# Kernel optimization log

Measured on AMD Instinct MI355X. Metric: run time of the kernel, lower is better.

The kernel has to match this reference:

```python
import jax, jax.numpy as jnp
import numpy as np

D_MODEL = 2048
NHEADS = 16
HEAD_DIM = D_MODEL // NHEADS


def setup_inputs() -> dict:
    key = jax.random.key(0)
    kx, kq, kk, kv, ko = jax.random.split(key, 5)
    B, S = 2, 2048
    scale = 1.0 / np.sqrt(D_MODEL)
    return {
        "x": jax.random.normal(kx, (B, S, D_MODEL), dtype=jnp.float32),
        "Wq": jax.random.normal(kq, (D_MODEL, D_MODEL), dtype=jnp.float32) * scale,
        "Wk": jax.random.normal(kk, (D_MODEL, D_MODEL), dtype=jnp.float32) * scale,
        "Wv": jax.random.normal(kv, (D_MODEL, D_MODEL), dtype=jnp.float32) * scale,
        "Wo": jax.random.normal(ko, (D_MODEL, D_MODEL), dtype=jnp.float32) * scale,
    }


def reference(x, Wq, Wk, Wv, Wo):
    B, S, _ = x.shape
    # nn.Linear(bias=False): y = x @ W.T
    q = (x @ Wq.T).reshape(B, S, NHEADS, HEAD_DIM)
    k = (x @ Wk.T).reshape(B, S, NHEADS, HEAD_DIM)
    v = (x @ Wv.T).reshape(B, S, NHEADS, HEAD_DIM)
    sm_scale = 1.0 / np.sqrt(HEAD_DIM)
    # scores: [B, H, S, S]
    scores = jnp.einsum("bqhd,bkhd->bhqk", q, k) * sm_scale
    causal_mask = jnp.tril(jnp.ones((S, S), dtype=bool))  # [S, S]
    scores = jnp.where(causal_mask, scores, jnp.finfo(scores.dtype).min)
    probs = jax.nn.softmax(scores, axis=-1)
    attn = jnp.einsum("bhqk,bkhd->bqhd", probs, v)  # [B, S, H, D]
    out = attn.reshape(B, S, D_MODEL) @ Wo.T
    return out
```

## Files before the change

kernel.cpp:

```cpp
#include <hip/hip_runtime.h>
#include <hip/hip_bf16.h>
#include <type_traits>

#define DEV __device__ __forceinline__

typedef __bf16 bf16x8 __attribute__((ext_vector_type(8)));
typedef float f32x4 __attribute__((ext_vector_type(4)));
typedef float f32x16 __attribute__((ext_vector_type(16)));
typedef unsigned short u16;
typedef unsigned int u32;

DEV u16 f32_to_bf16(float f) {
  union { float f; u32 u; } x; x.f = f;
  u32 r = (x.u + 0x7FFFu + ((x.u >> 16) & 1u)) >> 16;
  return (u16)r;
}

DEV u32 pack2(float a, float b) {
  union { __hip_bfloat162 h; u32 u; } c;
  c.h = __float22bfloat162_rn(float2{a, b});
  return c.u;
}

DEV void ld_lds16(const void* g, void* l) {
  __builtin_amdgcn_global_load_lds(
      (const __attribute__((address_space(1))) u32*)g,
      (__attribute__((address_space(3))) u32*)l, 16, 0, 0);
}

#define MFMA16(a, b, c) __builtin_amdgcn_mfma_f32_16x16x32_bf16(a, b, c, 0, 0, 0)
#define MFMA32(a, b, c) __builtin_amdgcn_mfma_f32_32x32x16_bf16(a, b, c, 0, 0, 0)

__global__ __launch_bounds__(256) void cast_all(
    const float* __restrict__ x,  const float* __restrict__ wq,
    const float* __restrict__ wk, const float* __restrict__ wv,
    const float* __restrict__ wo,
    u16* __restrict__ xb,  u16* __restrict__ wqb, u16* __restrict__ wkb,
    u16* __restrict__ wvb, u16* __restrict__ wob) {
  int bid = blockIdx.x;
  const float* src; u16* dst; int base;
  if (bid < 8192)       { src = x;  dst = xb;  base = bid; }
  else if (bid < 12288) { src = wq; dst = wqb; base = bid - 8192; }
  else if (bid < 16384) { src = wk; dst = wkb; base = bid - 12288; }
  else if (bid < 20480) { src = wv; dst = wvb; base = bid - 16384; }
  else                  { src = wo; dst = wob; base = bid - 20480; }
  int i = (base * 256 + threadIdx.x) * 4;
  float4 v = *reinterpret_cast<const float4*>(src + i);
  ushort4 o;
  o.x = f32_to_bf16(v.x); o.y = f32_to_bf16(v.y);
  o.z = f32_to_bf16(v.z); o.w = f32_to_bf16(v.w);
  *reinterpret_cast<ushort4*>(dst + i) = o;
}

template <typename OutT>
__global__ __launch_bounds__(512, 2) void gemm_nt256(
    const u16* __restrict__ A, const u16* __restrict__ B, OutT* __restrict__ C,
    int M, int N, int K, float oscLo, float oscHi, int nsplit, int nbx) {
  __shared__ __align__(16) u16 sA[2][256 * 64];
  __shared__ __align__(16) u16 sB[2][256 * 64];
  const int tid = threadIdx.x;
  const int lane = tid & 63, wid = tid >> 6;
  const int l31 = lane & 31, hi5 = lane >> 5;
  const int wm = wid >> 2, wn = wid & 3;
  const int cpx = gridDim.x >> 3;
  const int swz = ((int)blockIdx.x & 7) * cpx + ((int)blockIdx.x >> 3);
  const int m0 = (swz / nbx) * 256, n0 = (swz % nbx) * 256;
  const int NT = K >> 6;

  f32x16 acc[4][2] = {};

  auto stage = [&](int buf, int t) {
    const int k0 = t << 6;
#pragma unroll
    for (int i = 0; i < 4; ++i) {
      int e = i * 512 + tid;
      int r = e >> 3;
      int bc = ((e & 7) * 16) ^ ((r & 7) << 4);
      ld_lds16(A + (size_t)(m0 + r) * K + k0 + (bc >> 1), &sA[buf][e * 8]);
    }
#pragma unroll
    for (int i = 0; i < 4; ++i) {
      int e = i * 512 + tid;
      int r = e >> 3;
      int bc = ((e & 7) * 16) ^ ((r & 7) << 4);
      ld_lds16(B + (size_t)(n0 + r) * K + k0 + (bc >> 1), &sB[buf][e * 8]);
    }
  };

  stage(0, 0);
  __syncthreads();

  for (int t = 0; t < NT; ++t) {
    const u16* cA = sA[t & 1];
    const u16* cB = sB[t & 1];
    if (t + 1 < NT) stage((t + 1) & 1, t + 1);

#pragma unroll
    for (int kh = 0; kh < 2; ++kh) {
      bf16x8 afr[4][2], bfr[2][2];
#pragma unroll
      for (int mi = 0; mi < 4; ++mi)
#pragma unroll
        for (int kc = 0; kc < 2; ++kc) {
          int row = wm * 128 + mi * 32 + l31;
          int bo = (((kh * 2 + kc) * 32 + hi5 * 16)) ^ ((row & 7) << 4);
          afr[mi][kc] = *(const bf16x8*)((const char*)cA + row * 128 + bo);
        }
#pragma unroll
      for (int ni = 0; ni < 2; ++ni)
#pragma unroll
        for (int kc = 0; kc < 2; ++kc) {
          int row = wn * 64 + ni * 32 + l31;
          int bo = (((kh * 2 + kc) * 32 + hi5 * 16)) ^ ((row & 7) << 4);
          bfr[ni][kc] = *(const bf16x8*)((const char*)cB + row * 128 + bo);
        }
      asm volatile("s_waitcnt lgkmcnt(0)" ::: "memory");
      __builtin_amdgcn_sched_barrier(0);
      __builtin_amdgcn_s_setprio(1);
#pragma unroll
      for (int mi = 0; mi < 4; ++mi)
#pragma unroll
        for (int ni = 0; ni < 2; ++ni)
#pragma unroll
          for (int kc = 0; kc < 2; ++kc)
            acc[mi][ni] = MFMA32(afr[mi][kc], bfr[ni][kc], acc[mi][ni]);
      __builtin_amdgcn_s_setprio(0);
      __builtin_amdgcn_sched_barrier(0);
    }
    __syncthreads();
  }

#pragma unroll
  for (int mi = 0; mi < 4; ++mi)
#pragma unroll
    for (int ni = 0; ni < 2; ++ni) {
      int colb = n0 + wn * 64 + ni * 32;
      float osc = (colb < nsplit) ? oscLo : oscHi;
      int col = colb + l31;
#pragma unroll
      for (int j = 0; j < 16; ++j) {
        size_t row = m0 + wm * 128 + mi * 32 + (j & 3) + 8 * (j >> 2) + 4 * hi5;
        float v = acc[mi][ni][j] * osc;
        if constexpr (std::is_same<OutT, float>::value)
          C[row * N + col] = v;
        else
          C[row * N + col] = f32_to_bf16(v);
      }
    }
}

template <typename OutT>
__global__ __launch_bounds__(256) void gemm_nt(const u16* __restrict__ A,
                                               const u16* __restrict__ B,
                                               OutT* __restrict__ C,
                                               int M, int N, int K,
                                               float oscLo, float oscHi, int nsplit) {
  __shared__ __align__(16) u16 sA[128 * 64];
  __shared__ __align__(16) u16 sB[128 * 64];
  const int tid = threadIdx.x;
  const int lane = tid & 63, wid = tid >> 6;
  const int lo = lane & 15, hi = lane >> 4;
  const int wm = wid >> 1, wn = wid & 1;
  const int m0 = blockIdx.y * 128, n0 = blockIdx.x * 128;
  const float osc = (n0 < nsplit) ? oscLo : oscHi;

  f32x4 acc[4][4] = {};

  for (int k0 = 0; k0 < K; k0 += 64) {
    __syncthreads();
#pragma unroll
    for (int i = 0; i < 4; ++i) {
      int e16 = i * 256 + tid;
      int r = e16 >> 3;
      int bcol = ((e16 & 7) * 16) ^ ((r & 7) << 4);
      int col = bcol >> 1;
      ld_lds16(A + (size_t)(m0 + r) * K + k0 + col, sA + e16 * 8);
      ld_lds16(B + (size_t)(n0 + r) * K + k0 + col, sB + e16 * 8);
    }
    __syncthreads();
#pragma unroll
    for (int kc = 0; kc < 2; ++kc) {
      bf16x8 a[4], b[4];
#pragma unroll
      for (int i = 0; i < 4; ++i) {
        int row = wm * 64 + i * 16 + lo;
        int boff = ((kc * 32 + hi * 8) * 2) ^ ((row & 7) << 4);
        a[i] = *(const bf16x8*)((const char*)sA + row * 128 + boff);
      }
#pragma unroll
      for (int i = 0; i < 4; ++i) {
        int row = wn * 64 + i * 16 + lo;
        int boff = ((kc * 32 + hi * 8) * 2) ^ ((row & 7) << 4);
        b[i] = *(const bf16x8*)((const char*)sB + row * 128 + boff);
      }
#pragma unroll
      for (int mi = 0; mi < 4; ++mi)
#pragma unroll
        for (int ni = 0; ni < 4; ++ni)
          acc[mi][ni] = MFMA16(a[mi], b[ni], acc[mi][ni]);
    }
  }
#pragma unroll
  for (int mi = 0; mi < 4; ++mi)
#pragma unroll
    for (int r = 0; r < 4; ++r) {
      size_t row = m0 + wm * 64 + mi * 16 + hi * 4 + r;
#pragma unroll
      for (int ni = 0; ni < 4; ++ni) {
        int col = n0 + wn * 64 + ni * 16 + lo;
        float v = acc[mi][ni][r] * osc;
        if constexpr (std::is_same<OutT, float>::value)
          C[row * N + col] = v;
        else
          C[row * N + col] = f32_to_bf16(v);
      }
    }
}

constexpr float RTHR2 = 11.5416f;

__global__ __launch_bounds__(256, 2) void attn_fwd(const u16* __restrict__ QK,
                                                   const u16* __restrict__ VT,
                                                   u16* __restrict__ O) {
  __shared__ __align__(16) u16 sK[2][64 * 128];
  __shared__ __align__(16) u16 sV[2][128 * 64];

  const int x = blockIdx.x, h = blockIdx.y, b = blockIdx.z;
  const int qt = b ? x : (15 - x);
  const int tid = threadIdx.x;
  const int lane = tid & 63, wid = tid >> 6;
  const int l31 = lane & 31, hi5 = lane >> 5;

  const size_t baseQ = ((size_t)b * 2048) * 4096 + (size_t)h * 128;
  const size_t baseK = baseQ + 2048;
  const size_t baseV = ((size_t)h * 128) * 4096 + (size_t)b * 2048;
  const int q0 = qt * 128;
  const int qw = q0 + wid * 32;
  const int qg = qw + l31;
  const int nt = 2 * qt + 2;

  bf16x8 qf[8];
#pragma unroll
  for (int kc = 0; kc < 8; ++kc)
    qf[kc] = *(const bf16x8*)(QK + baseQ + (size_t)qg * 4096 + kc * 16 + hi5 * 8);

  f32x16 o[4] = {};
  float m = -INFINITY, ls = 0.f;

  auto stage = [&](int buf, int t) {
    const int kv = t * 64;
#pragma unroll
    for (int i = 0; i < 4; ++i) {
      int e = i * 256 + tid;
      int r = e >> 4;
      int bc = ((e & 15) * 16) ^ ((r & 7) << 4);
      ld_lds16(QK + baseK + (size_t)(kv + r) * 4096 + (bc >> 1), &sK[buf][e * 8]);
    }
#pragma unroll
    for (int i = 0; i < 4; ++i) {
      int e = i * 256 + tid;
      int r = e >> 3;
      int bc = ((e & 7) * 16) ^ ((r & 7) << 4);
      ld_lds16(VT + baseV + (size_t)r * 4096 + kv + (bc >> 1), &sV[buf][e * 8]);
    }
  };

  stage(0, 0);

  for (int t = 0; t < nt; ++t) {
    __syncthreads();
    if (t + 1 < nt) stage((t + 1) & 1, t + 1);
    const int kv0 = t * 64;
    if (kv0 > qw + 31) continue;
    const u16* bK = sK[t & 1];
    const u16* bV = sV[t & 1];

    f32x16 s[2] = {};
#pragma unroll
    for (int kb = 0; kb < 2; ++kb) {
      int row = kb * 32 + l31;
      int rsw = (row & 7) << 4;
#pragma unroll
      for (int kc = 0; kc < 8; ++kc) {
        int bo = (kc * 32 + hi5 * 16) ^ rsw;
        bf16x8 kf = *(const bf16x8*)((const char*)bK + row * 256 + bo);
        s[kb] = MFMA32(kf, qf[kc], s[kb]);
      }
    }

    if (kv0 + 63 > qw) {
#pragma unroll
      for (int kb = 0; kb < 2; ++kb)
#pragma unroll
        for (int j = 0; j < 16; ++j) {
          int keyg = kv0 + kb * 32 + (j & 3) + 8 * (j >> 2) + 4 * hi5;
          s[kb][j] = (keyg > qg) ? -3e38f : s[kb][j];
        }
    }

    float pmax = -3e38f;
#pragma unroll
    for (int kb = 0; kb < 2; ++kb)
#pragma unroll
      for (int j = 0; j < 16; ++j) pmax = fmaxf(pmax, s[kb][j]);
    pmax = fmaxf(pmax, __shfl_xor(pmax, 32));

    if (!__all(pmax - m <= RTHR2)) {
      float mn = fmaxf(m, pmax);
      float fr = exp2f(m - mn);
      ls *= fr;
#pragma unroll
      for (int d = 0; d < 4; ++d) o[d] *= fr;
      m = mn;
    }

    float rs = 0.f;
#pragma unroll
    for (int kb = 0; kb < 2; ++kb)
#pragma unroll
      for (int j = 0; j < 16; ++j) {
        float pv = exp2f(s[kb][j] - m);
        s[kb][j] = pv;
        rs += pv;
      }
    rs += __shfl_xor(rs, 32);
    ls += rs;

    union PF { u32 w[4]; bf16x8 v; };
    PF pf[4];
#pragma unroll
    for (int kb = 0; kb < 2; ++kb)
#pragma unroll
      for (int gp = 0; gp < 2; ++gp) {
        u32 keep[2], send[2];
#pragma unroll
        for (int w = 0; w < 2; ++w) {
          int ja = 8 * gp + 2 * w;
          int jb = 8 * gp + 4 + 2 * w;
          u32 aa = pack2(s[kb][ja], s[kb][ja + 1]);
          u32 bb = pack2(s[kb][jb], s[kb][jb + 1]);
          keep[w] = hi5 ? bb : aa;
          send[w] = hi5 ? aa : bb;
        }
        u32 recv0 = (u32)__shfl_xor((int)send[0], 32);
        u32 recv1 = (u32)__shfl_xor((int)send[1], 32);
        PF& f = pf[2 * kb + gp];
        f.w[0] = hi5 ? recv0 : keep[0];
        f.w[1] = hi5 ? recv1 : keep[1];
        f.w[2] = hi5 ? keep[0] : recv0;
        f.w[3] = hi5 ? keep[1] : recv1;
      }

#pragma unroll
    for (int d = 0; d < 4; ++d) {
      int row = d * 32 + l31;
      int rsw = (row & 7) << 4;
#pragma unroll
      for (int ks = 0; ks < 4; ++ks) {
        int bo = (ks * 32 + hi5 * 16) ^ rsw;
        bf16x8 vf = *(const bf16x8*)((const char*)bV + row * 128 + bo);
        o[d] = MFMA32(vf, pf[ks].v, o[d]);
      }
    }
  }

  float inv = 1.f / ls;
  size_t orow = (size_t)b * 2048 + qg;
#pragma unroll
  for (int d = 0; d < 4; ++d)
#pragma unroll
    for (int G = 0; G < 4; ++G) {
      union { u32 u[2]; ushort4 s4; } st;
      st.u[0] = pack2(o[d][4 * G + 0] * inv, o[d][4 * G + 1] * inv);
      st.u[1] = pack2(o[d][4 * G + 2] * inv, o[d][4 * G + 3] * inv);
      int col = h * 128 + d * 32 + 8 * G + 4 * hi5;
      *(ushort4*)(O + orow * 2048 + col) = st.s4;
    }
}

extern "C" void kernel_launch(void* const* d_in, const int* in_sizes, int n_in,
                              void* d_out, int out_size, void* d_ws, size_t ws_size,
                              hipStream_t stream) {
  const float* x  = (const float*)d_in[0];
  const float* Wq = (const float*)d_in[1];
  const float* Wk = (const float*)d_in[2];
  const float* Wv = (const float*)d_in[3];
  const float* Wo = (const float*)d_in[4];
  float* out = (float*)d_out;

  constexpr int B = 2, S = 2048, D = 2048;
  constexpr int M = B * S;
  constexpr float QSC = 0.12751742f;

  char* ws = (char*)d_ws;
  u16* xb  = (u16*)ws; ws += (size_t)M * D * 2;
  u16* wqb = (u16*)ws; ws += (size_t)D * D * 2;
  u16* wkb = (u16*)ws; ws += (size_t)D * D * 2;
  u16* wvb = (u16*)ws; ws += (size_t)D * D * 2;
  u16* wob = (u16*)ws; ws += (size_t)D * D * 2;
  u16* qk  = (u16*)ws; ws += (size_t)M * 2 * D * 2;
  u16* vT  = (u16*)ws; ws += (size_t)M * D * 2;
  u16* att = (u16*)ws; ws += (size_t)M * D * 2;

  cast_all<<<24576, 256, 0, stream>>>(x, Wq, Wk, Wv, Wo, xb, wqb, wkb, wvb, wob);

  gemm_nt256<u16><<<256, 512, 0, stream>>>(xb, wqb, qk, M, 2 * D, D,
                                           QSC, 1.0f, D, 16);
  gemm_nt<u16><<<dim3(M / 128, D / 128), 256, 0, stream>>>(wvb, xb, vT, D, M, D,
                                                           1.0f, 1.0f, 1 << 30);

  attn_fwd<<<dim3(16, 16, B), 256, 0, stream>>>(qk, vT, att);

  gemm_nt<float><<<dim3(D / 128, M / 128), 256, 0, stream>>>(att, wob, out, M, D, D,
                                                             1.0f, 1.0f, 1 << 30);
}
```

Baseline: 261.4 us.

## Split Q/K outputs and use vmcnt-based partial waits in 256-tile GEMM

The 256x256 GEMM loop swaps the full __syncthreads for an explicit s_waitcnt vmcnt(8) plus a raw s_barrier. The intent is to wait only for the current tile's async LDS loads while the next tile's loads stay in flight, which should hide more global-load latency. The fused Q/K projection now writes to two separate contiguous buffers with a 2048 row stride instead of one interleaved 4096-wide buffer. The attention kernel reads Q and K from those buffers, which may help locality. The correctness of the vmcnt(8) count depends on each stage issuing exactly 8 loads per thread.

```diff
diff --git a/kernel.cpp b/kernel.cpp
--- a/kernel.cpp
+++ b/kernel.cpp
@@ -54,8 +54,10 @@
 
 template <typename OutT>
 __global__ __launch_bounds__(512, 2) void gemm_nt256(
-    const u16* __restrict__ A, const u16* __restrict__ B, OutT* __restrict__ C,
-    int M, int N, int K, float oscLo, float oscHi, int nsplit, int nbx) {
+    const u16* __restrict__ A, const u16* __restrict__ B,
+    OutT* __restrict__ C, OutT* __restrict__ C2,
+    int M, int N, int K, int ldc,
+    float oscLo, float oscHi, int nsplit, int nbx) {
   __shared__ __align__(16) u16 sA[2][256 * 64];
   __shared__ __align__(16) u16 sB[2][256 * 64];
   const int tid = threadIdx.x;
@@ -88,12 +90,18 @@
   };
 
   stage(0, 0);
-  __syncthreads();
 
   for (int t = 0; t < NT; ++t) {
     const u16* cA = sA[t & 1];
     const u16* cB = sB[t & 1];
-    if (t + 1 < NT) stage((t + 1) & 1, t + 1);
+    if (t + 1 < NT) {
+      stage((t + 1) & 1, t + 1);
+      asm volatile("s_waitcnt vmcnt(8)" ::: "memory");
+    } else {
+      asm volatile("s_waitcnt vmcnt(0)" ::: "memory");
+    }
+    __builtin_amdgcn_s_barrier();
+    __builtin_amdgcn_sched_barrier(0);
 
 #pragma unroll
     for (int kh = 0; kh < 2; ++kh) {
@@ -127,7 +135,8 @@
       __builtin_amdgcn_s_setprio(0);
       __builtin_amdgcn_sched_barrier(0);
     }
-    __syncthreads();
+    __builtin_amdgcn_s_barrier();
+    __builtin_amdgcn_sched_barrier(0);
   }
 
 #pragma unroll
@@ -135,16 +144,18 @@
 #pragma unroll
     for (int ni = 0; ni < 2; ++ni) {
       int colb = n0 + wn * 64 + ni * 32;
-      float osc = (colb < nsplit) ? oscLo : oscHi;
-      int col = colb + l31;
+      bool lo_side = (colb < nsplit);
+      OutT* dst = lo_side ? C : C2;
+      float osc = lo_side ? oscLo : oscHi;
+      int col = (lo_side ? colb : colb - nsplit) + l31;
 #pragma unroll
       for (int j = 0; j < 16; ++j) {
         size_t row = m0 + wm * 128 + mi * 32 + (j & 3) + 8 * (j >> 2) + 4 * hi5;
         float v = acc[mi][ni][j] * osc;
         if constexpr (std::is_same<OutT, float>::value)
-          C[row * N + col] = v;
+          dst[row * ldc + col] = v;
         else
-          C[row * N + col] = f32_to_bf16(v);
+          dst[row * ldc + col] = f32_to_bf16(v);
       }
     }
 }
@@ -153,8 +164,7 @@
 __global__ __launch_bounds__(256) void gemm_nt(const u16* __restrict__ A,
                                                const u16* __restrict__ B,
                                                OutT* __restrict__ C,
-                                               int M, int N, int K,
-                                               float oscLo, float oscHi, int nsplit) {
+                                               int M, int N, int K, float osc) {
   __shared__ __align__(16) u16 sA[128 * 64];
   __shared__ __align__(16) u16 sB[128 * 64];
   const int tid = threadIdx.x;
@@ -162,7 +172,6 @@
   const int lo = lane & 15, hi = lane >> 4;
   const int wm = wid >> 1, wn = wid & 1;
   const int m0 = blockIdx.y * 128, n0 = blockIdx.x * 128;
-  const float osc = (n0 < nsplit) ? oscLo : oscHi;
 
   f32x4 acc[4][4] = {};
 
@@ -219,7 +228,8 @@
 
 constexpr float RTHR2 = 11.5416f;
 
-__global__ __launch_bounds__(256, 2) void attn_fwd(const u16* __restrict__ QK,
+__global__ __launch_bounds__(256, 2) void attn_fwd(const u16* __restrict__ Q,
+                                                   const u16* __restrict__ K,
                                                    const u16* __restrict__ VT,
                                                    u16* __restrict__ O) {
   __shared__ __align__(16) u16 sK[2][64 * 128];
@@ -231,9 +241,8 @@
   const int lane = tid & 63, wid = tid >> 6;
   const int l31 = lane & 31, hi5 = lane >> 5;
 
-  const size_t baseQ = ((size_t)b * 2048) * 4096 + (size_t)h * 128;
-  const size_t baseK = baseQ + 2048;
-  const size_t baseV = ((size_t)h * 128) * 4096 + (size_t)b * 2048;
+  const size_t baseQK = ((size_t)b * 2048) * 2048 + (size_t)h * 128;
+  const size_t baseV  = ((size_t)h * 128) * 4096 + (size_t)b * 2048;
   const int q0 = qt * 128;
   const int qw = q0 + wid * 32;
   const int qg = qw + l31;
@@ -242,7 +251,7 @@
   bf16x8 qf[8];
 #pragma unroll
   for (int kc = 0; kc < 8; ++kc)
-    qf[kc] = *(const bf16x8*)(QK + baseQ + (size_t)qg * 4096 + kc * 16 + hi5 * 8);
+    qf[kc] = *(const bf16x8*)(Q + baseQK + (size_t)qg * 2048 + kc * 16 + hi5 * 8);
 
   f32x16 o[4] = {};
   float m = -INFINITY, ls = 0.f;
@@ -254,7 +263,7 @@
       int e = i * 256 + tid;
       int r = e >> 4;
       int bc = ((e & 15) * 16) ^ ((r & 7) << 4);
-      ld_lds16(QK + baseK + (size_t)(kv + r) * 4096 + (bc >> 1), &sK[buf][e * 8]);
+      ld_lds16(K + baseQK + (size_t)(kv + r) * 2048 + (bc >> 1), &sK[buf][e * 8]);
     }
 #pragma unroll
     for (int i = 0; i < 4; ++i) {
@@ -398,19 +407,18 @@
   u16* wkb = (u16*)ws; ws += (size_t)D * D * 2;
   u16* wvb = (u16*)ws; ws += (size_t)D * D * 2;
   u16* wob = (u16*)ws; ws += (size_t)D * D * 2;
-  u16* qk  = (u16*)ws; ws += (size_t)M * 2 * D * 2;
+  u16* q   = (u16*)ws; ws += (size_t)M * D * 2;
+  u16* k   = (u16*)ws; ws += (size_t)M * D * 2;
   u16* vT  = (u16*)ws; ws += (size_t)M * D * 2;
   u16* att = (u16*)ws; ws += (size_t)M * D * 2;
 
   cast_all<<<24576, 256, 0, stream>>>(x, Wq, Wk, Wv, Wo, xb, wqb, wkb, wvb, wob);
 
-  gemm_nt256<u16><<<256, 512, 0, stream>>>(xb, wqb, qk, M, 2 * D, D,
+  gemm_nt256<u16><<<256, 512, 0, stream>>>(xb, wqb, q, k, M, 2 * D, D, D,
                                            QSC, 1.0f, D, 16);
-  gemm_nt<u16><<<dim3(M / 128, D / 128), 256, 0, stream>>>(wvb, xb, vT, D, M, D,
-                                                           1.0f, 1.0f, 1 << 30);
-
-  attn_fwd<<<dim3(16, 16, B), 256, 0, stream>>>(qk, vT, att);
-
-  gemm_nt<float><<<dim3(D / 128, M / 128), 256, 0, stream>>>(att, wob, out, M, D, D,
-                                                             1.0f, 1.0f, 1 << 30);
-}
+  gemm_nt<u16><<<dim3(M / 128, D / 128), 256, 0, stream>>>(wvb, xb, vT, D, M, D, 1.0f);
+
+  attn_fwd<<<dim3(16, 16, B), 256, 0, stream>>>(q, k, vT, att);
+
+  gemm_nt<float><<<dim3(D / 128, M / 128), 256, 0, stream>>>(att, wob, out, M, D, D, 1.0f);
+}
```

Measured after the change: 259.2 us. Within noise of the previous version (-0.8%).
